# Kernel tuning notes

Hardware: AMD Instinct MI355X
Metric: run time of the kernel (lower is better)

Reference implementation:

```python
import jax, jax.numpy as jnp
import numpy as np

NEG_INF = -1e30

def setup_inputs() -> dict:
    key = jax.random.key(0)
    k1, k2, k3 = jax.random.split(key, 3)
    B, H, S, D = 2, 16, 2048, 128
    q = jax.random.normal(k1, (B, H, S, D), dtype=jnp.float32)
    k = jax.random.normal(k2, (B, H, S, D), dtype=jnp.float32)
    v = jax.random.normal(k3, (B, H, S, D), dtype=jnp.float32)
    return {"q": q, "k": k, "v": v}

def reference(q, k, v):
    # F.scaled_dot_product_attention(q, k, v, is_causal=True), MATH backend:
    # full score matrix, causal mask (top-left aligned: j <= i), softmax, bmm.
    D = q.shape[-1]
    scale = 1.0 / jnp.sqrt(jnp.asarray(D, dtype=q.dtype))
    scores = jnp.einsum('bhqd,bhkd->bhqk', q, k) * scale  # [B,H,S,S]
    Sq, Sk = scores.shape[-2], scores.shape[-1]
    causal = jnp.arange(Sk)[None, :] <= jnp.arange(Sq)[:, None]  # [Sq,Sk]
    scores = jnp.where(causal[None, None], scores, NEG_INF)
    attn = jax.nn.softmax(scores, axis=-1)
    return jnp.einsum('bhqk,bhkd->bhqd', attn, v)
```

## Files before the change

### kernel.cpp

```cpp
#include <hip/hip_runtime.h>
#include <cstdint>
#include <cstddef>

typedef __attribute__((ext_vector_type(8))) short short8;
typedef __attribute__((ext_vector_type(4))) float floatx4;
typedef __attribute__((ext_vector_type(2))) unsigned int uint2v;

namespace {
constexpr int kBH  = 32;
constexpr int kS   = 2048;
constexpr int kD   = 128;
constexpr int kBQ  = 64;
constexpr int kBK  = 64;
constexpr int kNQT = kS / kBQ;
constexpr int PST  = 72;
constexpr size_t kKVElems = (size_t)kBH * kS * kD;
}

__device__ __forceinline__ unsigned cvt_pk_bf16(float lo, float hi) {
    unsigned r;
    asm("v_cvt_pk_bf16_f32 %0, %1, %2" : "=v"(r) : "v"(lo), "v"(hi));
    return r;
}

__device__ __forceinline__ unsigned pack_bf16x2(float lo, float hi) {
    return cvt_pk_bf16(lo, hi);
}

__device__ __forceinline__ float fast_exp2(float x) {
#if __has_builtin(__builtin_amdgcn_exp2f)
    return __builtin_amdgcn_exp2f(x);
#else
    return __expf(x * 0.6931471805599453f);
#endif
}

__global__ __launch_bounds__(256)
void prepass(const float* __restrict__ K, const float* __restrict__ V,
             unsigned short* __restrict__ Kb, unsigned short* __restrict__ Vt) {
    const int b = (int)blockIdx.x;
    const int t = (int)threadIdx.x;
    if (b < 4096) {
        const size_t i0 = ((size_t)b * 256 + t) * 8;
        floatx4 a = *(const floatx4*)(K + i0);
        floatx4 c = *(const floatx4*)(K + i0 + 4);
        union { unsigned u[4]; short8 v; } pk;
        pk.u[0] = cvt_pk_bf16(a[0], a[1]);
        pk.u[1] = cvt_pk_bf16(a[2], a[3]);
        pk.u[2] = cvt_pk_bf16(c[0], c[1]);
        pk.u[3] = cvt_pk_bf16(c[2], c[3]);
        *(short8*)(Kb + i0) = pk.v;
    } else {
        __shared__ float ldsT[64][68];
        const int vb = b - 4096;
        const int bh = vb >> 6;
        const int rem = vb & 63;
        const int s0 = (rem >> 1) * 64;
        const int d0 = (rem & 1) * 64;
        const float* vbase = V + ((size_t)bh * kS + s0) * kD + d0;
        const int sr = t >> 4, c4 = (t & 15) * 4;
#pragma unroll
        for (int p = 0; p < 4; ++p) {
            const int s = p * 16 + sr;
            *(floatx4*)&ldsT[s][c4] = *(const floatx4*)(vbase + (size_t)s * kD + c4);
        }
        __syncthreads();
        const int dr = t >> 2, sc = (t & 3) * 16;
        union { unsigned u[8]; short8 v[2]; } pk;
#pragma unroll
        for (int j = 0; j < 8; ++j)
            pk.u[j] = cvt_pk_bf16(ldsT[sc + 2 * j][dr], ldsT[sc + 2 * j + 1][dr]);
        unsigned short* out = Vt + ((size_t)(bh * kD + d0 + dr)) * kS + s0 + sc;
        *(short8*)out = pk.v[0];
        *(short8*)(out + 8) = pk.v[1];
    }
}

__device__ __forceinline__ short8 p_gather(unsigned pe0, unsigned pe1,
                                           unsigned po0, unsigned po1,
                                           int lane, int prm_lo, int prm_hi) {
    int ce0 = __builtin_amdgcn_ds_bpermute(prm_lo, (int)pe0);
    int ce1 = __builtin_amdgcn_ds_bpermute(prm_lo, (int)pe1);
    int ce2 = __builtin_amdgcn_ds_bpermute(prm_hi, (int)pe0);
    int ce3 = __builtin_amdgcn_ds_bpermute(prm_hi, (int)pe1);
    int co0 = __builtin_amdgcn_ds_bpermute(prm_lo, (int)po0);
    int co1 = __builtin_amdgcn_ds_bpermute(prm_lo, (int)po1);
    int co2 = __builtin_amdgcn_ds_bpermute(prm_hi, (int)po0);
    int co3 = __builtin_amdgcn_ds_bpermute(prm_hi, (int)po1);
    const bool hi = lane >= 32;
    union { unsigned u[4]; short8 v; } r;
    r.u[0] = hi ? (unsigned)co0 : (unsigned)ce0;
    r.u[1] = hi ? (unsigned)co1 : (unsigned)ce1;
    r.u[2] = hi ? (unsigned)co2 : (unsigned)ce2;
    r.u[3] = hi ? (unsigned)co3 : (unsigned)ce3;
    return r.v;
}

__global__ __launch_bounds__(512, 4)
void fa_fwd_ws(const float* __restrict__ Qg, const unsigned short* __restrict__ Kb,
               const unsigned short* __restrict__ Vt, float* __restrict__ Og) {
    const int id = (int)blockIdx.x;
    const int qA = id >> 5;
    const int qB = kNQT - 1 - qA;
    const int bh = (id & 7) * 4 + ((id >> 3) & 3);
    const int t    = (int)threadIdx.x;
    const int wave = t >> 6;
    const int g    = wave >> 2;
    const int wsub = wave & 3;
    const int lane = t & 63;
    const int quad = lane >> 4;
    const int l16  = lane & 15;
    const int qt   = g ? qB : qA;
    const int rowq = wsub * 16 + l16;
    const int prm_lo = (((lane >> 4) & 1) << 7) + (l16 << 2);
    const int prm_hi = prm_lo + 64;

    __shared__ __align__(16) unsigned short kT[kBK * 128];
    __shared__ __align__(16) unsigned short vT[kD * 64];

    const float scale = 0.12751744459649126f;

    short8  qf[4];
    floatx4 oacc[8];
    float   lsum = 0.f;
#pragma unroll
    for (int i = 0; i < 8; ++i) oacc[i] = (floatx4){0, 0, 0, 0};

    {
        const float* qp = Qg + ((size_t)bh * kS + qt * kBQ + wsub * 16 + l16) * kD;
#pragma unroll
        for (int ks = 0; ks < 4; ++ks) {
            const int d0 = ks * 32 + quad * 8;
            floatx4 a0 = *(const floatx4*)(qp + d0);
            floatx4 a1 = *(const floatx4*)(qp + d0 + 4);
            union { unsigned u[4]; short8 v; } pa;
            pa.u[0] = cvt_pk_bf16(a0[0] * scale, a0[1] * scale);
            pa.u[1] = cvt_pk_bf16(a0[2] * scale, a0[3] * scale);
            pa.u[2] = cvt_pk_bf16(a1[0] * scale, a1[1] * scale);
            pa.u[3] = cvt_pk_bf16(a1[2] * scale, a1[3] * scale);
            qf[ks] = pa.v;
        }
    }

    const unsigned short* kBase = Kb + (size_t)bh * kS * kD;
    const unsigned short* vBase = Vt + (size_t)bh * kD * kS;

    short8 stK[2], stV[2];
    const int krow0 = wave * 8 + (lane >> 4);
    const int kcg   = (lane & 15);
    const int vd0   = wave * 16 + (lane >> 3);
    const int vcg   = (lane & 7);

    auto issue = [&](int kt) {
        const int kj0 = kt * kBK;
#pragma unroll
        for (int i = 0; i < 2; ++i) {
            const int row = krow0 + i * 4;
            const int cg  = kcg ^ (row & 15);
            stK[i] = *(const short8*)(kBase + ((size_t)(kj0 + row)) * kD + cg * 8);
        }
#pragma unroll
        for (int i = 0; i < 2; ++i) {
            const int d  = vd0 + i * 8;
            const int cg = vcg ^ (d & 7);
            stV[i] = *(const short8*)(vBase + (size_t)d * kS + kj0 + cg * 8);
        }
    };
    auto write_lds = [&]() {
#pragma unroll
        for (int i = 0; i < 2; ++i)
            *(short8*)&kT[(wave * 8 + i * 4) * 128 + lane * 8] = stK[i];
#pragma unroll
        for (int i = 0; i < 2; ++i)
            *(short8*)&vT[(wave * 16 + i * 8) * 64 + lane * 8] = stV[i];
    };

    auto tile_step = [&](bool doMask) {
        floatx4 sacc[4];
        __builtin_amdgcn_s_setprio(1);
#pragma unroll
        for (int nt = 0; nt < 4; ++nt) {
            floatx4 acc = (floatx4){0.f, 0.f, 0.f, 0.f};
#pragma unroll
            for (int ks = 0; ks < 4; ++ks) {
                short8 kf = *(const short8*)&kT[(nt * 16 + l16) * 128 + (((ks * 4 + quad) ^ l16) << 3)];
                acc = __builtin_amdgcn_mfma_f32_16x16x32_bf16(kf, qf[ks], acc, 0, 0, 0);
            }
            sacc[nt] = acc;
        }
        __builtin_amdgcn_s_setprio(0);

        float ls = 0.f;
#pragma unroll
        for (int nt = 0; nt < 4; ++nt)
#pragma unroll
            for (int r = 0; r < 4; ++r) {
                float e = fast_exp2(sacc[nt][r]);
                if (doMask && (nt * 16 + quad * 4 + r > rowq)) e = 0.f;
                sacc[nt][r] = e;
                ls += e;
            }
        lsum += ls;

        unsigned pk[4][2];
#pragma unroll
        for (int nt = 0; nt < 4; ++nt) {
            pk[nt][0] = cvt_pk_bf16(sacc[nt][0], sacc[nt][1]);
            pk[nt][1] = cvt_pk_bf16(sacc[nt][2], sacc[nt][3]);
        }
        short8 pf[2];
        pf[0] = p_gather(pk[0][0], pk[0][1], pk[1][0], pk[1][1], lane, prm_lo, prm_hi);
        pf[1] = p_gather(pk[2][0], pk[2][1], pk[3][0], pk[3][1], lane, prm_lo, prm_hi);

        __builtin_amdgcn_s_setprio(1);
#pragma unroll
        for (int nd = 0; nd < 8; ++nd) {
            floatx4 acc = oacc[nd];
#pragma unroll
            for (int ks = 0; ks < 2; ++ks) {
                short8 vf = *(const short8*)&vT[(nd * 16 + l16) * 64 + ((((ks * 4 + quad)) ^ (l16 & 7)) << 3)];
                acc = __builtin_amdgcn_mfma_f32_16x16x32_bf16(pf[ks], vf, acc, 0, 0, 0);
            }
            oacc[nd] = acc;
        }
        __builtin_amdgcn_s_setprio(0);
    };

    issue(0);
    write_lds();
    asm volatile("s_waitcnt lgkmcnt(0)" ::: "memory");
    __builtin_amdgcn_s_barrier();
    __builtin_amdgcn_sched_barrier(0);

    for (int kt = 0;; ++kt) {
        if (kt < qB) issue(kt + 1);
        if (kt <= qt) tile_step(kt == qt);
        if (kt == qB) break;
        asm volatile("" ::: "memory");
        __builtin_amdgcn_s_barrier();
        __builtin_amdgcn_sched_barrier(0);
        write_lds();
        asm volatile("s_waitcnt lgkmcnt(0)" ::: "memory");
        __builtin_amdgcn_s_barrier();
        __builtin_amdgcn_sched_barrier(0);
    }

    float rs = lsum;
    rs += __shfl_xor(rs, 16, 64);
    rs += __shfl_xor(rs, 32, 64);
    float inv[4];
#pragma unroll
    for (int r = 0; r < 4; ++r)
        inv[r] = 1.0f / __shfl(rs, quad * 4 + r, 64);
    float* ob = Og + ((size_t)bh * kS + qt * kBQ + wsub * 16 + quad * 4) * kD;
#pragma unroll
    for (int nd = 0; nd < 8; ++nd)
#pragma unroll
        for (int r = 0; r < 4; ++r)
            ob[(size_t)r * kD + nd * 16 + l16] = oacc[nd][r] * inv[r];
}

namespace {
constexpr int kBKf = 64;
constexpr int KSTf = 136;
constexpr int VSTf = 72;
}

struct TileStateF {
    short8  qf[4];
    floatx4 oacc[8];
    float   lsum[4];
};

__device__ __forceinline__ void tile_step_f(
    TileStateF& ts, const unsigned short* kT, const unsigned short* vT,
    unsigned short* pw, int l16, int quad, int rowl, bool doMask)
{
    floatx4 sacc[4];
    __builtin_amdgcn_s_setprio(1);
#pragma unroll
    for (int nt = 0; nt < 4; ++nt) {
        floatx4 acc = (floatx4){0.f, 0.f, 0.f, 0.f};
#pragma unroll
        for (int ks = 0; ks < 4; ++ks) {
            short8 kf = *(const short8*)&kT[(nt * 16 + l16) * KSTf + ks * 32 + quad * 8];
            acc = __builtin_amdgcn_mfma_f32_16x16x32_bf16(ts.qf[ks], kf, acc, 0, 0, 0);
        }
        sacc[nt] = acc;
    }
    __builtin_amdgcn_s_setprio(0);
    if (doMask) {
#pragma unroll
        for (int nt = 0; nt < 4; ++nt) {
            const int col = nt * 16 + l16;
#pragma unroll
            for (int r = 0; r < 4; ++r)
                if (col > rowl + r) sacc[nt][r] = -1e30f;
        }
    }
#pragma unroll
    for (int nt = 0; nt < 4; ++nt)
#pragma unroll
        for (int r = 0; r < 4; ++r)
            sacc[nt][r] = fast_exp2(sacc[nt][r]);
#pragma unroll
    for (int r = 0; r < 4; ++r)
        ts.lsum[r] += (sacc[0][r] + sacc[1][r]) + (sacc[2][r] + sacc[3][r]);
#pragma unroll
    for (int r = 0; r < 4; ++r) {
#pragma unroll
        for (int np = 0; np < 2; ++np) {
            const unsigned u = cvt_pk_bf16(sacc[np * 2][r], sacc[np * 2 + 1][r]);
            pw[(quad * 4 + r) * PST + (np * 2) * 16 + l16]     = (unsigned short)u;
            pw[(quad * 4 + r) * PST + (np * 2 + 1) * 16 + l16] = (unsigned short)(u >> 16);
        }
    }
    short8 pf[2];
#pragma unroll
    for (int ks = 0; ks < 2; ++ks)
        pf[ks] = *(const short8*)&pw[l16 * PST + ks * 32 + quad * 8];
    __builtin_amdgcn_s_setprio(1);
#pragma unroll
    for (int nd = 0; nd < 8; ++nd) {
        floatx4 acc = ts.oacc[nd];
#pragma unroll
        for (int ks = 0; ks < 2; ++ks) {
            short8 vf = *(const short8*)&vT[(nd * 16 + l16) * VSTf + ks * 32 + quad * 8];
            acc = __builtin_amdgcn_mfma_f32_16x16x32_bf16(pf[ks], vf, acc, 0, 0, 0);
        }
        ts.oacc[nd] = acc;
    }
    __builtin_amdgcn_s_setprio(0);
}

__global__ __launch_bounds__(256, 2)
void fa_fwd_fallback(const float* __restrict__ Qg, const float* __restrict__ Kg,
                     const float* __restrict__ Vg, float* __restrict__ Og) {
    const int id = (int)blockIdx.x;
    const int qA = id >> 5;
    const int qB = kNQT - 1 - qA;
    const int bh = id & (kBH - 1);
    const int t    = (int)threadIdx.x;
    const int wave = t >> 6;
    const int lane = t & 63;
    const int quad = lane >> 4;
    const int l16  = lane & 15;
    const int rowl = wave * 16 + quad * 4;

    __shared__ __align__(16) unsigned short kT[2][kBKf * KSTf];
    __shared__ __align__(16) unsigned short vT[2][kD * VSTf];
    __shared__ __align__(16) unsigned short pT[4 * 16 * PST];
    unsigned short* pw = &pT[wave * 16 * PST];

    const float scale = 0.12751744459649126f;

    TileStateF A, B;
#pragma unroll
    for (int i = 0; i < 8; ++i) { A.oacc[i] = (floatx4){0,0,0,0}; B.oacc[i] = (floatx4){0,0,0,0}; }
#pragma unroll
    for (int r = 0; r < 4; ++r) { A.lsum[r] = 0.f; B.lsum[r] = 0.f; }
    {
        const float* qpA = Qg + ((size_t)bh * kS + qA * kBQ + wave * 16 + l16) * kD;
        const float* qpB = Qg + ((size_t)bh * kS + qB * kBQ + wave * 16 + l16) * kD;
#pragma unroll
        for (int ks = 0; ks < 4; ++ks) {
            const int d0 = ks * 32 + quad * 8;
            floatx4 a0 = *(const floatx4*)(qpA + d0);
            floatx4 a1 = *(const floatx4*)(qpA + d0 + 4);
            floatx4 b0 = *(const floatx4*)(qpB + d0);
            floatx4 b1 = *(const floatx4*)(qpB + d0 + 4);
            union { unsigned u[4]; short8 v; } pa, pb;
            pa.u[0] = cvt_pk_bf16(a0[0] * scale, a0[1] * scale);
            pa.u[1] = cvt_pk_bf16(a0[2] * scale, a0[3] * scale);
            pa.u[2] = cvt_pk_bf16(a1[0] * scale, a1[1] * scale);
            pa.u[3] = cvt_pk_bf16(a1[2] * scale, a1[3] * scale);
            pb.u[0] = cvt_pk_bf16(b0[0] * scale, b0[1] * scale);
            pb.u[1] = cvt_pk_bf16(b0[2] * scale, b0[3] * scale);
            pb.u[2] = cvt_pk_bf16(b1[0] * scale, b1[1] * scale);
            pb.u[3] = cvt_pk_bf16(b1[2] * scale, b1[3] * scale);
            A.qf[ks] = pa.v;
            B.qf[ks] = pb.v;
        }
    }

    const int kRow8 = t >> 5;
    const int kCol4 = t & 31;
    const int vD    = t & 127;
    const int vR2   = t >> 7;
    const float* kBaseH = Kg + (size_t)bh * kS * kD;
    const float* vBaseH = Vg + (size_t)bh * kS * kD;
    floatx4 kpre[8];
    float   vpreL[16], vpreH[16];

    auto issue_kv_loads = [&](int kt) {
        const float* kb = kBaseH + (size_t)(kt * kBKf) * kD;
        const float* vb = vBaseH + (size_t)(kt * kBKf) * kD;
#pragma unroll
        for (int p = 0; p < 8; ++p)
            kpre[p] = *(const floatx4*)(kb + (size_t)(p * 8 + kRow8) * kD + kCol4 * 4);
#pragma unroll
        for (int p = 0; p < 16; ++p) {
            const int j = p * 2 + vR2;
            vpreL[p] = vb[(size_t)(2 * j) * kD + vD];
            vpreH[p] = vb[(size_t)(2 * j + 1) * kD + vD];
        }
    };
    auto store_kv = [&](int buf) {
#pragma unroll
        for (int p = 0; p < 8; ++p) {
            union { unsigned u[2]; uint2v v; } w;
            w.u[0] = cvt_pk_bf16(kpre[p][0], kpre[p][1]);
            w.u[1] = cvt_pk_bf16(kpre[p][2], kpre[p][3]);
            *(uint2v*)&kT[buf][(p * 8 + kRow8) * KSTf + kCol4 * 4] = w.v;
        }
#pragma unroll
        for (int p = 0; p < 16; ++p) {
            const int j = p * 2 + vR2;
            *(unsigned*)&vT[buf][vD * VSTf + 2 * j] = pack_bf16x2(vpreL[p], vpreH[p]);
        }
    };

    const int last = qB;
    issue_kv_loads(0);
    store_kv(0);
    __syncthreads();
    for (int kt = 0; kt <= last; ++kt) {
        const int buf = kt & 1;
        if (kt < last) issue_kv_loads(kt + 1);
        if (kt <= qA) tile_step_f(A, kT[buf], vT[buf], pw, l16, quad, rowl, kt == qA);
        tile_step_f(B, kT[buf], vT[buf], pw, l16, quad, rowl, kt == last);
        if (kt < last) {
            store_kv(buf ^ 1);
            __syncthreads();
        }
    }
#pragma unroll
    for (int tile = 0; tile < 2; ++tile) {
        TileStateF& ts = tile ? B : A;
        const int qt = tile ? qB : qA;
        float ls[4];
#pragma unroll
        for (int r = 0; r < 4; ++r) ls[r] = ts.lsum[r];
#pragma unroll
        for (int off = 1; off < 16; off <<= 1)
#pragma unroll
            for (int r = 0; r < 4; ++r)
                ls[r] += __shfl_xor(ls[r], off, 64);
        float inv[4];
#pragma unroll
        for (int r = 0; r < 4; ++r) inv[r] = 1.0f / ls[r];
        float* ob = Og + ((size_t)bh * kS + qt * kBQ + wave * 16 + quad * 4) * kD;
#pragma unroll
        for (int nd = 0; nd < 8; ++nd)
#pragma unroll
            for (int r = 0; r < 4; ++r)
                ob[(size_t)r * kD + nd * 16 + l16] = ts.oacc[nd][r] * inv[r];
    }
}

extern "C" void kernel_launch(void* const* d_in, const int* in_sizes, int n_in,
                              void* d_out, int out_size, void* d_ws, size_t ws_size,
                              hipStream_t stream) {
    (void)in_sizes; (void)n_in; (void)out_size;
    const float* q = (const float*)d_in[0];
    const float* k = (const float*)d_in[1];
    const float* v = (const float*)d_in[2];
    float* o = (float*)d_out;
    const size_t need = 2 * kKVElems * sizeof(unsigned short);
    if (ws_size >= need) {
        unsigned short* Kb = (unsigned short*)d_ws;
        unsigned short* Vt = Kb + kKVElems;
        prepass<<<dim3(4096 + 2048), 256, 0, stream>>>(k, v, Kb, Vt);
        fa_fwd_ws<<<dim3((kNQT / 2) * kBH), 512, 0, stream>>>(q, Kb, Vt, o);
    } else {
        fa_fwd_fallback<<<dim3((kNQT / 2) * kBH), 256, 0, stream>>>(q, k, v, o);
    }
}
```

Baseline: 181.3 us.

## Switch attention kernel to 32x32x16 MFMA with 4 waves per block

Replaces the 16x16x32 bf16 MFMA tiling with 32x32x16 MFMA, so each wave owns 32 query rows and the block shrinks from 8 to 4 waves. The P-matrix relayout moves from eight ds_bpermute ops per fragment to v_permlane32_swap register swaps, and each thread issues twice as many K/V staging loads. The larger MFMA shape is meant to raise matrix throughput per LDS read and to remove LDS-routed permutes. In exchange, accumulator register pressure rises, with fewer waves for latency hiding and launch bounds lowered to 2 blocks per SM.

```diff
diff --git a/kernel.cpp b/kernel.cpp
--- a/kernel.cpp
+++ b/kernel.cpp
@@ -4,6 +4,7 @@
 
 typedef __attribute__((ext_vector_type(8))) short short8;
 typedef __attribute__((ext_vector_type(4))) float floatx4;
+typedef __attribute__((ext_vector_type(16))) float floatx16;
 typedef __attribute__((ext_vector_type(2))) unsigned int uint2v;
 
 namespace {
@@ -76,27 +77,8 @@
     }
 }
 
-__device__ __forceinline__ short8 p_gather(unsigned pe0, unsigned pe1,
-                                           unsigned po0, unsigned po1,
-                                           int lane, int prm_lo, int prm_hi) {
-    int ce0 = __builtin_amdgcn_ds_bpermute(prm_lo, (int)pe0);
-    int ce1 = __builtin_amdgcn_ds_bpermute(prm_lo, (int)pe1);
-    int ce2 = __builtin_amdgcn_ds_bpermute(prm_hi, (int)pe0);
-    int ce3 = __builtin_amdgcn_ds_bpermute(prm_hi, (int)pe1);
-    int co0 = __builtin_amdgcn_ds_bpermute(prm_lo, (int)po0);
-    int co1 = __builtin_amdgcn_ds_bpermute(prm_lo, (int)po1);
-    int co2 = __builtin_amdgcn_ds_bpermute(prm_hi, (int)po0);
-    int co3 = __builtin_amdgcn_ds_bpermute(prm_hi, (int)po1);
-    const bool hi = lane >= 32;
-    union { unsigned u[4]; short8 v; } r;
-    r.u[0] = hi ? (unsigned)co0 : (unsigned)ce0;
-    r.u[1] = hi ? (unsigned)co1 : (unsigned)ce1;
-    r.u[2] = hi ? (unsigned)co2 : (unsigned)ce2;
-    r.u[3] = hi ? (unsigned)co3 : (unsigned)ce3;
-    return r.v;
-}
-
-__global__ __launch_bounds__(512, 4)
+
+__global__ __launch_bounds__(256, 2)
 void fa_fwd_ws(const float* __restrict__ Qg, const unsigned short* __restrict__ Kb,
                const unsigned short* __restrict__ Vt, float* __restrict__ Og) {
     const int id = (int)blockIdx.x;
@@ -105,62 +87,61 @@
     const int bh = (id & 7) * 4 + ((id >> 3) & 3);
     const int t    = (int)threadIdx.x;
     const int wave = t >> 6;
-    const int g    = wave >> 2;
-    const int wsub = wave & 3;
+    const int g    = wave >> 1;
+    const int half = wave & 1;
     const int lane = t & 63;
-    const int quad = lane >> 4;
-    const int l16  = lane & 15;
+    const int l31  = lane & 31;
+    const int hl   = lane >> 5;
     const int qt   = g ? qB : qA;
-    const int rowq = wsub * 16 + l16;
-    const int prm_lo = (((lane >> 4) & 1) << 7) + (l16 << 2);
-    const int prm_hi = prm_lo + 64;
+    const int rowq = half * 32 + l31;
 
     __shared__ __align__(16) unsigned short kT[kBK * 128];
     __shared__ __align__(16) unsigned short vT[kD * 64];
 
     const float scale = 0.12751744459649126f;
 
-    short8  qf[4];
-    floatx4 oacc[8];
-    float   lsum = 0.f;
-#pragma unroll
-    for (int i = 0; i < 8; ++i) oacc[i] = (floatx4){0, 0, 0, 0};
+    short8   qf[8];
+    floatx16 oacc[4];
+    float    lsum = 0.f;
+#pragma unroll
+    for (int i = 0; i < 4; ++i)
+        oacc[i] = (floatx16){0,0,0,0,0,0,0,0,0,0,0,0,0,0,0,0};
 
     {
-        const float* qp = Qg + ((size_t)bh * kS + qt * kBQ + wsub * 16 + l16) * kD;
-#pragma unroll
-        for (int ks = 0; ks < 4; ++ks) {
-            const int d0 = ks * 32 + quad * 8;
-            floatx4 a0 = *(const floatx4*)(qp + d0);
-            floatx4 a1 = *(const floatx4*)(qp + d0 + 4);
+        const float* qp = Qg + ((size_t)bh * kS + qt * 64 + half * 32 + l31) * kD;
+#pragma unroll
+        for (int s = 0; s < 8; ++s) {
+            const int c = (2 * s + hl) * 8;
+            floatx4 a0 = *(const floatx4*)(qp + c);
+            floatx4 a1 = *(const floatx4*)(qp + c + 4);
             union { unsigned u[4]; short8 v; } pa;
             pa.u[0] = cvt_pk_bf16(a0[0] * scale, a0[1] * scale);
             pa.u[1] = cvt_pk_bf16(a0[2] * scale, a0[3] * scale);
             pa.u[2] = cvt_pk_bf16(a1[0] * scale, a1[1] * scale);
             pa.u[3] = cvt_pk_bf16(a1[2] * scale, a1[3] * scale);
-            qf[ks] = pa.v;
+            qf[s] = pa.v;
         }
     }
 
     const unsigned short* kBase = Kb + (size_t)bh * kS * kD;
     const unsigned short* vBase = Vt + (size_t)bh * kD * kS;
 
-    short8 stK[2], stV[2];
-    const int krow0 = wave * 8 + (lane >> 4);
-    const int kcg   = (lane & 15);
-    const int vd0   = wave * 16 + (lane >> 3);
-    const int vcg   = (lane & 7);
+    short8 stK[4], stV[4];
+    const int krow0 = wave * 16 + (lane >> 4);
+    const int kcg   = lane & 15;
+    const int vd0   = wave * 32 + (lane >> 3);
+    const int vcg   = lane & 7;
 
     auto issue = [&](int kt) {
         const int kj0 = kt * kBK;
 #pragma unroll
-        for (int i = 0; i < 2; ++i) {
+        for (int i = 0; i < 4; ++i) {
             const int row = krow0 + i * 4;
             const int cg  = kcg ^ (row & 15);
             stK[i] = *(const short8*)(kBase + ((size_t)(kj0 + row)) * kD + cg * 8);
         }
 #pragma unroll
-        for (int i = 0; i < 2; ++i) {
+        for (int i = 0; i < 4; ++i) {
             const int d  = vd0 + i * 8;
             const int cg = vcg ^ (d & 7);
             stV[i] = *(const short8*)(vBase + (size_t)d * kS + kj0 + cg * 8);
@@ -168,60 +149,71 @@
     };
     auto write_lds = [&]() {
 #pragma unroll
-        for (int i = 0; i < 2; ++i)
-            *(short8*)&kT[(wave * 8 + i * 4) * 128 + lane * 8] = stK[i];
-#pragma unroll
-        for (int i = 0; i < 2; ++i)
-            *(short8*)&vT[(wave * 16 + i * 8) * 64 + lane * 8] = stV[i];
+        for (int i = 0; i < 4; ++i)
+            *(short8*)&kT[(wave * 16 + i * 4) * 128 + lane * 8] = stK[i];
+#pragma unroll
+        for (int i = 0; i < 4; ++i)
+            *(short8*)&vT[(wave * 32 + i * 8) * 64 + lane * 8] = stV[i];
     };
 
     auto tile_step = [&](bool doMask) {
-        floatx4 sacc[4];
+        floatx16 sacc[2];
         __builtin_amdgcn_s_setprio(1);
 #pragma unroll
-        for (int nt = 0; nt < 4; ++nt) {
-            floatx4 acc = (floatx4){0.f, 0.f, 0.f, 0.f};
-#pragma unroll
-            for (int ks = 0; ks < 4; ++ks) {
-                short8 kf = *(const short8*)&kT[(nt * 16 + l16) * 128 + (((ks * 4 + quad) ^ l16) << 3)];
-                acc = __builtin_amdgcn_mfma_f32_16x16x32_bf16(kf, qf[ks], acc, 0, 0, 0);
+        for (int kk = 0; kk < 2; ++kk) {
+            floatx16 acc = (floatx16){0,0,0,0,0,0,0,0,0,0,0,0,0,0,0,0};
+#pragma unroll
+            for (int s = 0; s < 8; ++s) {
+                short8 kf = *(const short8*)&kT[(kk * 32 + l31) * 128 + (((2 * s + hl) ^ (lane & 15)) << 3)];
+                acc = __builtin_amdgcn_mfma_f32_32x32x16_bf16(kf, qf[s], acc, 0, 0, 0);
             }
-            sacc[nt] = acc;
+            sacc[kk] = acc;
         }
         __builtin_amdgcn_s_setprio(0);
 
         float ls = 0.f;
 #pragma unroll
-        for (int nt = 0; nt < 4; ++nt)
-#pragma unroll
-            for (int r = 0; r < 4; ++r) {
-                float e = fast_exp2(sacc[nt][r]);
-                if (doMask && (nt * 16 + quad * 4 + r > rowq)) e = 0.f;
-                sacc[nt][r] = e;
+        for (int kk = 0; kk < 2; ++kk)
+#pragma unroll
+            for (int r = 0; r < 16; ++r) {
+                float e = fast_exp2(sacc[kk][r]);
+                if (doMask && (kk * 32 + (r & 3) + 8 * (r >> 2) + 4 * hl > rowq)) e = 0.f;
+                sacc[kk][r] = e;
                 ls += e;
             }
         lsum += ls;
 
-        unsigned pk[4][2];
-#pragma unroll
-        for (int nt = 0; nt < 4; ++nt) {
-            pk[nt][0] = cvt_pk_bf16(sacc[nt][0], sacc[nt][1]);
-            pk[nt][1] = cvt_pk_bf16(sacc[nt][2], sacc[nt][3]);
-        }
-        short8 pf[2];
-        pf[0] = p_gather(pk[0][0], pk[0][1], pk[1][0], pk[1][1], lane, prm_lo, prm_hi);
-        pf[1] = p_gather(pk[2][0], pk[2][1], pk[3][0], pk[3][1], lane, prm_lo, prm_hi);
+        unsigned pk[2][8];
+#pragma unroll
+        for (int kk = 0; kk < 2; ++kk)
+#pragma unroll
+            for (int i = 0; i < 8; ++i)
+                pk[kk][i] = cvt_pk_bf16(sacc[kk][2 * i], sacc[kk][2 * i + 1]);
+
+        short8 pf[4];
+#pragma unroll
+        for (int kk = 0; kk < 2; ++kk)
+#pragma unroll
+            for (int sub = 0; sub < 2; ++sub) {
+                unsigned a0 = pk[kk][4 * sub + 0], a1 = pk[kk][4 * sub + 1];
+                unsigned b0 = pk[kk][4 * sub + 2], b1 = pk[kk][4 * sub + 3];
+                asm("v_permlane32_swap_b32 %0, %1" : "+v"(a0), "+v"(b0));
+                asm("v_permlane32_swap_b32 %0, %1" : "+v"(a1), "+v"(b1));
+                union { unsigned u[4]; short8 v; } w;
+                w.u[0] = a0; w.u[1] = a1; w.u[2] = b0; w.u[3] = b1;
+                pf[kk * 2 + sub] = w.v;
+            }
 
         __builtin_amdgcn_s_setprio(1);
 #pragma unroll
-        for (int nd = 0; nd < 8; ++nd) {
-            floatx4 acc = oacc[nd];
-#pragma unroll
-            for (int ks = 0; ks < 2; ++ks) {
-                short8 vf = *(const short8*)&vT[(nd * 16 + l16) * 64 + ((((ks * 4 + quad)) ^ (l16 & 7)) << 3)];
-                acc = __builtin_amdgcn_mfma_f32_16x16x32_bf16(pf[ks], vf, acc, 0, 0, 0);
+        for (int db = 0; db < 4; ++db) {
+            floatx16 acc = oacc[db];
+#pragma unroll
+            for (int ks = 0; ks < 4; ++ks) {
+                short8 vf = *(const short8*)&vT[(db * 32 + l31) * 64 + (((2 * ks + hl) ^ (lane & 7)) << 3)];
+                acc = __builtin_amdgcn_mfma_f32_32x32x16_bf16(pf[ks], vf, acc, 0, 0, 0);
             }
-            oacc[nd] = acc;
+            oacc[db] = acc;
         }
         __builtin_amdgcn_s_setprio(0);
     };
@@ -246,18 +238,17 @@
     }
 
     float rs = lsum;
-    rs += __shfl_xor(rs, 16, 64);
     rs += __shfl_xor(rs, 32, 64);
-    float inv[4];
-#pragma unroll
-    for (int r = 0; r < 4; ++r)
-        inv[r] = 1.0f / __shfl(rs, quad * 4 + r, 64);
-    float* ob = Og + ((size_t)bh * kS + qt * kBQ + wsub * 16 + quad * 4) * kD;
-#pragma unroll
-    for (int nd = 0; nd < 8; ++nd)
-#pragma unroll
-        for (int r = 0; r < 4; ++r)
-            ob[(size_t)r * kD + nd * 16 + l16] = oacc[nd][r] * inv[r];
+    const float inv_all = 1.0f / rs;
+    float* ob = Og + ((size_t)bh * kS + qt * 64 + half * 32) * kD;
+#pragma unroll
+    for (int db = 0; db < 4; ++db)
+#pragma unroll
+        for (int r = 0; r < 16; ++r) {
+            const int qrow = (r & 3) + 8 * (r >> 2) + 4 * hl;
+            const float inv = __shfl(inv_all, qrow, 64);
+            ob[(size_t)qrow * kD + db * 32 + l31] = oacc[db][r] * inv;
+        }
 }
 
 namespace {
@@ -471,7 +462,7 @@
         unsigned short* Kb = (unsigned short*)d_ws;
         unsigned short* Vt = Kb + kKVElems;
         prepass<<<dim3(4096 + 2048), 256, 0, stream>>>(k, v, Kb, Vt);
-        fa_fwd_ws<<<dim3((kNQT / 2) * kBH), 512, 0, stream>>>(q, Kb, Vt, o);
+        fa_fwd_ws<<<dim3((kNQT / 2) * kBH), 256, 0, stream>>>(q, Kb, Vt, o);
     } else {
         fa_fwd_fallback<<<dim3((kNQT / 2) * kBH), 256, 0, stream>>>(q, k, v, o);
     }
```

After: 185.6 us. 1.02x slower.
